# Optimization experiments

Hardware: AMD Instinct MI355X
Metric: run time of the kernel (lower is better)

## Reference

```python
import jax, jax.numpy as jnp
import numpy as np

N, E, D, Z, EA = 25000, 400000, 32, 128, 4


def _mlp(h, W1, b1, W2, b2):
    # MLP_ALL_ACT: activation after every Linear layer
    h = jax.nn.relu(h @ W1 + b1)
    return jax.nn.relu(h @ W2 + b2)


def _super_edge_conv(x, src, dst, edge_attr,
                     eW1, eb1, eW2, eb2, lW1, lb1, lW2, lb2, residual):
    xi = x[dst]            # [E, F] target node features (PyG x_i)
    xj = x[src]            # [E, F] source node features (PyG x_j)
    d = xj - xi
    p = xj * xi
    e1 = jnp.linalg.norm(d, axis=-1, keepdims=True)   # [E, 1]
    e2 = jnp.sum(p, axis=-1, keepdims=True)           # [E, 1]
    feat = jnp.concatenate([xi, d, p, e1, e2, edge_attr], axis=-1)  # [E, 3F+2+EA]
    m = _mlp(feat, eW1, eb1, eW2, eb2)                # [E, Z]
    agg = jax.ops.segment_max(m, dst, num_segments=x.shape[0])  # max aggr per dst node
    agg = jnp.where(jnp.isfinite(agg), agg, 0.0)      # PyG fills empty segments with 0
    y = _mlp(jnp.concatenate([x, agg], axis=-1), lW1, lb1, lW2, lb2)
    return y + x if residual else y


def setup_inputs() -> dict:
    key = jax.random.key(0)
    keys = iter(jax.random.split(key, 64))

    def xav(din, dout):
        s = float(np.sqrt(2.0 / (din + dout)))
        return jax.random.normal(next(keys), (din, dout), jnp.float32) * s

    inp = {}
    inp["x"] = jax.random.normal(next(keys), (N, D), jnp.float32)
    inp["edge_index"] = jax.random.randint(next(keys), (2, E), 0, N)
    inp["edge_attr"] = jax.random.normal(next(keys), (E, EA), jnp.float32)

    def conv_params(prefix, fin):
        e_in = 3 * fin + 2 + EA
        inp[prefix + "_eW1"] = xav(e_in, Z); inp[prefix + "_eb1"] = jnp.zeros((Z,), jnp.float32)
        inp[prefix + "_eW2"] = xav(Z, Z);    inp[prefix + "_eb2"] = jnp.zeros((Z,), jnp.float32)
        inp[prefix + "_lW1"] = xav(fin + Z, Z); inp[prefix + "_lb1"] = jnp.zeros((Z,), jnp.float32)
        inp[prefix + "_lW2"] = xav(Z, Z);    inp[prefix + "_lb2"] = jnp.zeros((Z,), jnp.float32)

    conv_params("c1", D)
    conv_params("c2", Z)
    conv_params("c3", Z)
    inp["fus_W1"] = xav(3 * Z, 2 * Z); inp["fus_b1"] = jnp.zeros((2 * Z,), jnp.float32)
    inp["fus_W2"] = xav(2 * Z, Z);     inp["fus_b2"] = jnp.zeros((Z,), jnp.float32)
    return inp


def reference(x, edge_index, edge_attr,
              c1_eW1, c1_eb1, c1_eW2, c1_eb2, c1_lW1, c1_lb1, c1_lW2, c1_lb2,
              c2_eW1, c2_eb1, c2_eW2, c2_eb2, c2_lW1, c2_lb1, c2_lW2, c2_lb2,
              c3_eW1, c3_eb1, c3_eW2, c3_eb2, c3_lW1, c3_lb1, c3_lW2, c3_lb2,
              fus_W1, fus_b1, fus_W2, fus_b2):
    src, dst = edge_index[0], edge_index[1]
    x1 = _super_edge_conv(x, src, dst, edge_attr,
                          c1_eW1, c1_eb1, c1_eW2, c1_eb2,
                          c1_lW1, c1_lb1, c1_lW2, c1_lb2, residual=False)
    x2 = _super_edge_conv(x1, src, dst, edge_attr,
                          c2_eW1, c2_eb1, c2_eW2, c2_eb2,
                          c2_lW1, c2_lb1, c2_lW2, c2_lb2, residual=True)
    x3 = _super_edge_conv(x2, src, dst, edge_attr,
                          c3_eW1, c3_eb1, c3_eW2, c3_eb2,
                          c3_lW1, c3_lb1, c3_lW2, c3_lb2, residual=True)
    return _mlp(jnp.concatenate([x1, x2, x3], axis=-1), fus_W1, fus_b1, fus_W2, fus_b2)
```

## Files before the change

kernel.cpp:

```cpp
#include <hip/hip_runtime.h>
#include <math.h>

#define DEV __device__ __forceinline__

typedef __attribute__((ext_vector_type(8))) short bf16x8;
typedef __attribute__((ext_vector_type(4))) float f32x4;

DEV short f2bf(float v) {
    union { float f; unsigned u; } c; c.f = v;
    unsigned r = c.u + 0x7fffu + ((c.u >> 16) & 1u);
    return (short)(r >> 16);
}
DEV float bf2f(short s) {
    return __uint_as_float(((unsigned)(unsigned short)s) << 16);
}
DEV unsigned cvt_pk(float lo, float hi) {
    unsigned r;
    asm("v_cvt_pk_bf16_f32 %0, %1, %2" : "=v"(r) : "v"(lo), "v"(hi));
    return r;
}
DEV uint2 pk4(const float4 v) {
    uint2 r; r.x = cvt_pk(v.x, v.y); r.y = cvt_pk(v.z, v.w); return r;
}

#define NPACK 20
struct PackJobs {
    const float* W[NPACK];
    const float* Wsub[NPACK];
    int KIN[NPACK];
    int NOUT[NPACK];
    int end[NPACK];
};

__global__ __launch_bounds__(256)
void pack_all(PackJobs j, short* __restrict__ out, int total)
{
    const int idx = blockIdx.x * 256 + threadIdx.x;
    if (idx >= total) return;
    int job = 0;
    while (idx >= j.end[job]) ++job;
    const int base = job ? j.end[job - 1] : 0;
    const int w = idx - base;
    const int nout = j.NOUT[job];
    const int per_ks = nout * 32;
    const int ks = w / per_ks;
    const int r  = w - ks * per_ks;
    const int n  = r >> 5;
    const int kg = (r >> 3) & 3;
    const int i  = r & 7;
    const int k  = ks * 32 + kg * 8 + i;
    float val = 0.0f;
    if (k < j.KIN[job]) {
        val = j.W[job][(size_t)k * nout + n];
        if (j.Wsub[job]) val -= j.Wsub[job][(size_t)k * nout + n];
    }
    out[idx] = f2bf(val);
}

__global__ __launch_bounds__(256)
void hist_kernel(const int* __restrict__ dst, int* __restrict__ cnt, int E)
{
    const int e = blockIdx.x * 256 + threadIdx.x;
    if (e < E) atomicAdd(&cnt[dst[e]], 1);
}

__global__ __launch_bounds__(1024)
void scan_kernel(int* __restrict__ cnt, int NB)
{
    __shared__ int part[1024];
    const int t = threadIdx.x;
    const int CH = (NB + 1023) >> 10;
    const int base = t * CH;
    int s = 0;
    for (int k = 0; k < CH; ++k) { const int i = base + k; if (i < NB) s += cnt[i]; }
    part[t] = s;
    __syncthreads();
    for (int off = 1; off < 1024; off <<= 1) {
        const int add = (t >= off) ? part[t - off] : 0;
        __syncthreads();
        part[t] += add;
        __syncthreads();
    }
    int run = part[t] - s;
    for (int k = 0; k < CH; ++k) {
        const int i = base + k;
        if (i < NB) { const int c = cnt[i]; cnt[i] = run; run += c; }
    }
}

__global__ __launch_bounds__(256)
void scatter_kernel(const int* __restrict__ src, const int* __restrict__ dst,
                    const float* __restrict__ ea, int* __restrict__ cursor,
                    int* __restrict__ sSrc, int* __restrict__ sDst,
                    short* __restrict__ eaB, int E)
{
    const int e = blockIdx.x * 256 + threadIdx.x;
    if (e >= E) return;
    const int d = dst[e];
    const int p = atomicAdd(&cursor[d], 1);
    sSrc[p] = src[e];
    sDst[p] = d;
    const float4 a = ((const float4*)ea)[e];
    *(uint2*)(eaB + (size_t)p * 4) = pk4(a);
}

template<int KP, int FSTR, int NOUT, bool BIAS>
DEV void mfma_gemm(const short* aLds, const short* __restrict__ Wpk,
                   const float* __restrict__ b, int row0, int c0, int lane,
                   f32x4 (&acc)[8])
{
    const int l15 = lane & 15;
    const int lg  = lane >> 4;
#pragma unroll
    for (int f = 0; f < 8; ++f) {
        if (BIAS) {
            const float bv = b[c0 + f * 16 + l15];
            acc[f] = (f32x4){bv, bv, bv, bv};
        } else {
            acc[f] = (f32x4){0.f, 0.f, 0.f, 0.f};
        }
    }
    const short* arow  = aLds + (row0 + l15) * FSTR + lg * 8;
    const short* wbase = Wpk + (size_t)(c0 + l15) * 32 + lg * 8;
#pragma unroll
    for (int ks = 0; ks < KP / 32; ++ks) {
        const bf16x8 av = *(const bf16x8*)(arow + ks * 32);
        const short* wp = wbase + (size_t)ks * NOUT * 32;
#pragma unroll
        for (int f = 0; f < 8; ++f) {
            const bf16x8 bv = *(const bf16x8*)(wp + f * 512);
            acc[f] = __builtin_amdgcn_mfma_f32_16x16x32_bf16(av, bv, acc[f], 0, 0, 0);
        }
    }
}

template<int OSTR>
DEV void pack_relu(const f32x4 (&acc)[8], short* out, int row0, int c0, int lane)
{
    const int l15 = lane & 15;
    const int lg  = lane >> 4;
#pragma unroll
    for (int f = 0; f < 8; ++f)
#pragma unroll
        for (int i = 0; i < 4; ++i) {
            const int row = row0 + lg * 4 + i;
            const int col = c0 + f * 16 + l15;
            const float vv = fmaxf(acc[f][i], 0.0f);
            const float o = __shfl_xor(vv, 1);
            if (!(lane & 1))
                *(unsigned*)&out[row * OSTR + col] = cvt_pk(vv, o);
        }
}

DEV void store_bf16(const f32x4 (&acc)[8], short* __restrict__ out,
                    int n0, int wave, int lane, int N)
{
    const int l15 = lane & 15;
    const int lg  = lane >> 4;
#pragma unroll
    for (int f = 0; f < 8; ++f)
#pragma unroll
        for (int i = 0; i < 4; ++i) {
            const float vv = acc[f][i];
            const float o = __shfl_xor(vv, 1);
            if (!(lane & 1)) {
                const int n = n0 + wave * 16 + lg * 4 + i;
                if (n < N)
                    *(unsigned*)&out[(size_t)n * 128 + f * 16 + l15] = cvt_pk(vv, o);
            }
        }
}

template<int FIN, int FSTR>
__global__ __launch_bounds__(256)
void uv_pre(const float* __restrict__ xin,
            const short* __restrict__ Wd, const float* __restrict__ b1,
            const short* __restrict__ Wb,
            short* __restrict__ uB, short* __restrict__ vB,
            float* __restrict__ sq, short* __restrict__ xB, int N)
{
    __shared__ __align__(16) short feat[64 * FSTR];
    const int tid = threadIdx.x, lane = tid & 63, wave = tid >> 6;
    const int n0 = blockIdx.x * 64;
    {
        const int r = tid >> 2, s = tid & 3, n = n0 + r;
        short* frow = feat + r * FSTR;
        if (n < N) {
            const float4* xr = (const float4*)(xin + (size_t)n * FIN);
            float ss = 0.f;
#pragma unroll
            for (int d4 = s; d4 < FIN / 4; d4 += 4) {
                const float4 a = xr[d4];
                ss += a.x * a.x + a.y * a.y + a.z * a.z + a.w * a.w;
                const uint2 sv = pk4(a);
                *(uint2*)(frow + d4 * 4) = sv;
                *(uint2*)(xB + (size_t)n * FIN + d4 * 4) = sv;
            }
            ss += __shfl_xor(ss, 1); ss += __shfl_xor(ss, 2);
            if (s == 0) sq[n] = ss;
        } else {
            for (int d = s * 4; d < FIN; d += 16) *(short4*)(frow + d) = make_short4(0, 0, 0, 0);
        }
    }
    asm volatile("s_waitcnt lgkmcnt(0)" ::: "memory");
    f32x4 acc[8];
    mfma_gemm<FIN, FSTR, 128, true>(feat, Wd, b1, wave * 16, 0, lane, acc);
    store_bf16(acc, uB, n0, wave, lane, N);
    mfma_gemm<FIN, FSTR, 128, false>(feat, Wb, nullptr, wave * 16, 0, lane, acc);
    store_bf16(acc, vB, n0, wave, lane, N);
}

template<int FIN>
__global__ __launch_bounds__(512, 8)
void edge_conv7(const short* __restrict__ xB,
                const int* __restrict__ sSrc, const int* __restrict__ sDst,
                const short* __restrict__ eaB, const float* __restrict__ sq,
                const short* __restrict__ uB, const short* __restrict__ vB,
                const short* __restrict__ W1pk, const short* __restrict__ W2pk,
                const float* __restrict__ b2,
                float* __restrict__ agg, int E, int swzQ, int swzR)
{
    constexpr int KPP  = FIN + 32;
    constexpr int FSTR = KPP + 8;
    constexpr int H1STR = 136;
    __shared__ __align__(16) short feat[64 * FSTR];
    __shared__ __align__(16) short h1s[64 * H1STR];
    __shared__ int dstv[64];
    const int tid = threadIdx.x, lane = tid & 63, wave = tid >> 6;
    const int l15 = lane & 15, lg = lane >> 4;
    int bid = blockIdx.x;
    {
        const int xcd = bid & 7, idx = bid >> 3;
        bid = (xcd < swzR ? xcd * (swzQ + 1)
                          : swzR * (swzQ + 1) + (xcd - swzR) * swzQ) + idx;
    }
    const int e0 = bid * 64;
    const int c0 = wave * 16;

    {
        const int r = tid >> 3, s = tid & 7, e = e0 + r;
        short* frow = feat + r * FSTR;
        short* urow = h1s + r * H1STR;
        if (e < E) {
            const int si = sSrc[e], di = sDst[e];
            if (s == 0) dstv[r] = di;
            float sp = 0.f;
#pragma unroll
            for (int c = s; c < FIN / 8; c += 8) {
                const bf16x8 a = *(const bf16x8*)(xB + (size_t)si * FIN + c * 8);
                const bf16x8 b = *(const bf16x8*)(xB + (size_t)di * FIN + c * 8);
                float p[8];
#pragma unroll
                for (int jj = 0; jj < 8; ++jj) {
                    p[jj] = bf2f(a[jj]) * bf2f(b[jj]);
                    sp += p[jj];
                }
                uint4 w;
                w.x = cvt_pk(p[0], p[1]); w.y = cvt_pk(p[2], p[3]);
                w.z = cvt_pk(p[4], p[5]); w.w = cvt_pk(p[6], p[7]);
                *(uint4*)(frow + c * 8) = w;
            }
            sp += __shfl_xor(sp, 1); sp += __shfl_xor(sp, 2); sp += __shfl_xor(sp, 4);
            if (s == 0) {
                const float e1v = sqrtf(fmaxf(sq[si] + sq[di] - 2.f * sp, 0.f));
                *(unsigned*)(frow + FIN) = cvt_pk(e1v, sp);
            }
            if (s == 1) {
                const short4 ea = *(const short4*)(eaB + (size_t)e * 4);
                *(short2*)(frow + FIN + 2) = make_short2(ea.x, ea.y);
                *(short2*)(frow + FIN + 4) = make_short2(ea.z, ea.w);
            }
            for (int d = FIN + 6 + s; d < KPP; d += 8) frow[d] = 0;
#pragma unroll
            for (int c = s; c < 16; c += 8) {
                const bf16x8 uu = *(const bf16x8*)(uB + (size_t)di * 128 + c * 8);
                const bf16x8 vv = *(const bf16x8*)(vB + (size_t)si * 128 + c * 8);
                float o[8];
#pragma unroll
                for (int jj = 0; jj < 8; ++jj)
                    o[jj] = bf2f(uu[jj]) + bf2f(vv[jj]);
                uint4 w;
                w.x = cvt_pk(o[0], o[1]); w.y = cvt_pk(o[2], o[3]);
                w.z = cvt_pk(o[4], o[5]); w.w = cvt_pk(o[6], o[7]);
                *(uint4*)(urow + c * 8) = w;
            }
        } else {
            if (s == 0) dstv[r] = -1;
            for (int d = s * 4; d < KPP; d += 32) *(short4*)(frow + d) = make_short4(0, 0, 0, 0);
            for (int d = s * 4; d < 128; d += 32) *(short4*)(urow + d) = make_short4(0, 0, 0, 0);
        }
    }
    __syncthreads();

    f32x4 acc[4];
#pragma unroll
    for (int sb = 0; sb < 4; ++sb) acc[sb] = (f32x4){0.f, 0.f, 0.f, 0.f};
    {
        const short* wb = W1pk + (size_t)(c0 + l15) * 32 + lg * 8;
#pragma unroll
        for (int ks = 0; ks < KPP / 32; ++ks) {
            const bf16x8 bv = *(const bf16x8*)(wb + (size_t)ks * 4096);
#pragma unroll
            for (int sb = 0; sb < 4; ++sb) {
                const bf16x8 av =
                    *(const bf16x8*)(feat + (sb * 16 + l15) * FSTR + ks * 32 + lg * 8);
                acc[sb] = __builtin_amdgcn_mfma_f32_16x16x32_bf16(av, bv, acc[sb], 0, 0, 0);
            }
        }
    }
#pragma unroll
    for (int sb = 0; sb < 4; ++sb)
#pragma unroll
        for (int i = 0; i < 4; ++i) {
            const int row = sb * 16 + lg * 4 + i;
            const int col = c0 + l15;
            float vv = acc[sb][i] + bf2f(h1s[row * H1STR + col]);
            vv = fmaxf(vv, 0.0f);
            const float o = __shfl_xor(vv, 1);
            if (!(lane & 1))
                *(unsigned*)&h1s[row * H1STR + col] = cvt_pk(vv, o);
        }
    __syncthreads();

    {
        const float bv0 = b2[c0 + l15];
#pragma unroll
        for (int sb = 0; sb < 4; ++sb) acc[sb] = (f32x4){bv0, bv0, bv0, bv0};
    }
    {
        const short* wb = W2pk + (size_t)(c0 + l15) * 32 + lg * 8;
#pragma unroll
        for (int ks = 0; ks < 4; ++ks) {
            const bf16x8 bv = *(const bf16x8*)(wb + (size_t)ks * 4096);
#pragma unroll
            for (int sb = 0; sb < 4; ++sb) {
                const bf16x8 av =
                    *(const bf16x8*)(h1s + (sb * 16 + l15) * H1STR + ks * 32 + lg * 8);
                acc[sb] = __builtin_amdgcn_mfma_f32_16x16x32_bf16(av, bv, acc[sb], 0, 0, 0);
            }
        }
    }
    __syncthreads();

#pragma unroll
    for (int sb = 0; sb < 4; ++sb)
#pragma unroll
        for (int i = 0; i < 4; ++i) {
            const int row = sb * 16 + lg * 4 + i;
            const int col = c0 + l15;
            const float vv = fmaxf(acc[sb][i], 0.0f);
            const float o = __shfl_xor(vv, 1);
            if (!(lane & 1))
                *(unsigned*)&h1s[row * H1STR + col] = cvt_pk(vv, o);
        }
    __syncthreads();

    {
        const int c  = tid & 127;
        const int rh = tid >> 7;
        int cur = -1;
        float mx = 0.0f;
#pragma unroll 4
        for (int i2 = 0; i2 < 16; ++i2) {
            const int row = rh * 16 + i2;
            const int d = dstv[row];
            const float val = bf2f(h1s[row * H1STR + c]);
            if (d != cur) {
                if (cur >= 0 && mx > 0.f)
                    atomicMax((int*)agg + (size_t)cur * 128 + c, __float_as_int(mx));
                cur = d;
                mx = val;
            } else {
                mx = fmaxf(mx, val);
            }
        }
        if (cur >= 0 && mx > 0.f)
            atomicMax((int*)agg + (size_t)cur * 128 + c, __float_as_int(mx));
    }
}

template<int FIN, int KP, int FSTR, bool RES>
__global__ __launch_bounds__(256)
void node_mfma(const float* __restrict__ xin, const float* __restrict__ agg,
               const short* __restrict__ W1pk, const float* __restrict__ b1,
               const short* __restrict__ W2pk, const float* __restrict__ b2,
               float* __restrict__ out, int N)
{
    constexpr int H1STR = 136;
    __shared__ __align__(16) short sh[64 * FSTR + 64 * H1STR];
    short* feat = sh;
    short* h1s  = sh + 64 * FSTR;
    const int tid = threadIdx.x, lane = tid & 63, wave = tid >> 6;
    const int n0 = blockIdx.x * 64;

    {
        const int r = tid >> 2, s = tid & 3, n = n0 + r;
        short* frow = feat + r * FSTR;
        if (n < N) {
            const float4* xr = (const float4*)(xin + (size_t)n * FIN);
            const float4* ar = (const float4*)(agg + (size_t)n * 128);
#pragma unroll
            for (int d4 = s; d4 < FIN / 4; d4 += 4)
                *(uint2*)(frow + d4 * 4) = pk4(xr[d4]);
#pragma unroll
            for (int d4 = s; d4 < 32; d4 += 4)
                *(uint2*)(frow + FIN + d4 * 4) = pk4(ar[d4]);
        } else {
            for (int d = s * 4; d < KP; d += 16) *(short4*)(frow + d) = make_short4(0, 0, 0, 0);
        }
    }
    asm volatile("s_waitcnt lgkmcnt(0)" ::: "memory");

    f32x4 acc[8];
    mfma_gemm<KP, FSTR, 128, true>(feat, W1pk, b1, wave * 16, 0, lane, acc);
    pack_relu<H1STR>(acc, h1s, wave * 16, 0, lane);
    asm volatile("s_waitcnt lgkmcnt(0)" ::: "memory");
    mfma_gemm<128, H1STR, 128, true>(h1s, W2pk, b2, wave * 16, 0, lane, acc);
    {
        const int l15 = lane & 15, lg = lane >> 4;
#pragma unroll
        for (int f = 0; f < 8; ++f)
#pragma unroll
            for (int i = 0; i < 4; ++i) {
                const int n = n0 + wave * 16 + lg * 4 + i;
                if (n < N) {
                    const int c = f * 16 + l15;
                    float v = fmaxf(acc[f][i], 0.0f);
                    if (RES) v += xin[(size_t)n * 128 + c];
                    out[(size_t)n * 128 + c] = v;
                }
            }
    }
}

__global__ __launch_bounds__(128)
void fusion_mfma(const float* __restrict__ x1, const float* __restrict__ x2,
                 const float* __restrict__ x3,
                 const short* __restrict__ W1pk, const float* __restrict__ b1,
                 const short* __restrict__ W2pk, const float* __restrict__ b2,
                 float* __restrict__ out, int N)
{
    constexpr int FSTR = 392;
    constexpr int H1STR = 264;
    __shared__ __align__(16) short sh[32 * FSTR + 32 * H1STR];
    short* feat = sh;
    short* h1s  = sh + 32 * FSTR;
    const int tid = threadIdx.x, lane = tid & 63, wave = tid >> 6;
    const int n0 = blockIdx.x * 32;

    {
        const int r = tid >> 2, s = tid & 3, n = n0 + r;
        short* frow = feat + r * FSTR;
        if (n < N) {
            const float4* a1 = (const float4*)(x1 + (size_t)n * 128);
            const float4* a2 = (const float4*)(x2 + (size_t)n * 128);
            const float4* a3 = (const float4*)(x3 + (size_t)n * 128);
#pragma unroll
            for (int d4 = s; d4 < 32; d4 += 4) {
                *(uint2*)(frow + d4 * 4)       = pk4(a1[d4]);
                *(uint2*)(frow + 128 + d4 * 4) = pk4(a2[d4]);
                *(uint2*)(frow + 256 + d4 * 4) = pk4(a3[d4]);
            }
        } else {
            for (int d = s * 4; d < 384; d += 16) *(short4*)(frow + d) = make_short4(0, 0, 0, 0);
        }
    }
    asm volatile("s_waitcnt lgkmcnt(0)" ::: "memory");

    f32x4 acc[8];
#pragma unroll
    for (int c0 = 0; c0 < 256; c0 += 128) {
        mfma_gemm<384, FSTR, 256, true>(feat, W1pk, b1, wave * 16, c0, lane, acc);
        pack_relu<H1STR>(acc, h1s, wave * 16, c0, lane);
    }
    asm volatile("s_waitcnt lgkmcnt(0)" ::: "memory");
    mfma_gemm<256, H1STR, 128, true>(h1s, W2pk, b2, wave * 16, 0, lane, acc);
    {
        const int l15 = lane & 15, lg = lane >> 4;
#pragma unroll
        for (int f = 0; f < 8; ++f)
#pragma unroll
            for (int i = 0; i < 4; ++i) {
                const int n = n0 + wave * 16 + lg * 4 + i;
                if (n < N)
                    out[(size_t)n * 128 + f * 16 + l15] = fmaxf(acc[f][i], 0.0f);
            }
    }
}

extern "C" void kernel_launch(void* const* d_in, const int* in_sizes, int n_in,
                              void* d_out, int out_size, void* d_ws, size_t ws_size,
                              hipStream_t stream)
{
    const float* x    = (const float*)d_in[0];
    const int*   eidx = (const int*)d_in[1];
    const float* ea   = (const float*)d_in[2];

    const float* c1_eW1 = (const float*)d_in[3];
    const float* c1_eb1 = (const float*)d_in[4];
    const float* c1_eW2 = (const float*)d_in[5];
    const float* c1_eb2 = (const float*)d_in[6];
    const float* c1_lW1 = (const float*)d_in[7];
    const float* c1_lb1 = (const float*)d_in[8];
    const float* c1_lW2 = (const float*)d_in[9];
    const float* c1_lb2 = (const float*)d_in[10];

    const float* c2_eW1 = (const float*)d_in[11];
    const float* c2_eb1 = (const float*)d_in[12];
    const float* c2_eW2 = (const float*)d_in[13];
    const float* c2_eb2 = (const float*)d_in[14];
    const float* c2_lW1 = (const float*)d_in[15];
    const float* c2_lb1 = (const float*)d_in[16];
    const float* c2_lW2 = (const float*)d_in[17];
    const float* c2_lb2 = (const float*)d_in[18];

    const float* c3_eW1 = (const float*)d_in[19];
    const float* c3_eb1 = (const float*)d_in[20];
    const float* c3_eW2 = (const float*)d_in[21];
    const float* c3_eb2 = (const float*)d_in[22];
    const float* c3_lW1 = (const float*)d_in[23];
    const float* c3_lb1 = (const float*)d_in[24];
    const float* c3_lW2 = (const float*)d_in[25];
    const float* c3_lb2 = (const float*)d_in[26];

    const float* fus_W1 = (const float*)d_in[27];
    const float* fus_b1 = (const float*)d_in[28];
    const float* fus_W2 = (const float*)d_in[29];
    const float* fus_b2 = (const float*)d_in[30];

    const int N = in_sizes[0] / 32;
    const int E = in_sizes[1] / 2;
    const int* srcI = eidx;
    const int* dstI = eidx + E;

    const size_t NP = (size_t)N * 128;
    float* ws  = (float*)d_ws;
    float* x1  = ws;
    float* x2  = x1 + NP;
    float* x3  = x2 + NP;
    float* agg = x3 + NP;
    float* sq  = agg + NP;
    int* cursor = (int*)(sq + N);
    int* sSrc   = cursor + 25024;
    int* sDst   = sSrc + E;
    short* eaB  = (short*)(sDst + E);
    short* uB   = eaB + (size_t)E * 4;
    short* vB   = uB + NP;
    short* xB   = vB + NP;
    short* wpk  = xB + NP;

    short* e1Wd = wpk + 0;
    short* e1Wb = wpk + 4096;
    short* e1Wp = wpk + 8192;
    short* e1W2 = wpk + 16384;
    short* e2Wd = wpk + 32768;
    short* e2Wb = wpk + 49152;
    short* e2Wp = wpk + 65536;
    short* e2W2 = wpk + 86016;
    short* e3Wd = wpk + 102400;
    short* e3Wb = wpk + 118784;
    short* e3Wp = wpk + 135168;
    short* e3W2 = wpk + 155648;
    short* n1W1 = wpk + 172032;
    short* n1W2 = wpk + 192512;
    short* n2W1 = wpk + 208896;
    short* n2W2 = wpk + 241664;
    short* n3W1 = wpk + 258048;
    short* n3W2 = wpk + 290816;
    short* fW1  = wpk + 307200;
    short* fW2  = wpk + 405504;
    const int packTotal = 438272;

    PackJobs pj;
    const float* pw[NPACK] = {
        c1_eW1, c1_eW1 + 32 * 128, c1_eW1 + 64 * 128, c1_eW2,
        c2_eW1, c2_eW1 + 128 * 128, c2_eW1 + 256 * 128, c2_eW2,
        c3_eW1, c3_eW1 + 128 * 128, c3_eW1 + 256 * 128, c3_eW2,
        c1_lW1, c1_lW2, c2_lW1, c2_lW2, c3_lW1, c3_lW2,
        fus_W1, fus_W2};
    const float* ps[NPACK] = {
        c1_eW1 + 32 * 128, nullptr, nullptr, nullptr,
        c2_eW1 + 128 * 128, nullptr, nullptr, nullptr,
        c3_eW1 + 128 * 128, nullptr, nullptr, nullptr,
        nullptr, nullptr, nullptr, nullptr, nullptr, nullptr,
        nullptr, nullptr};
    const int pk_kin[NPACK]  = {32, 32, 38, 128, 128, 128, 134, 128,
                                128, 128, 134, 128, 160, 128, 256, 128, 256, 128,
                                384, 256};
    const int pk_nout[NPACK] = {128, 128, 128, 128, 128, 128, 128, 128,
                                128, 128, 128, 128, 128, 128, 128, 128, 128, 128,
                                256, 128};
    const int pk_end[NPACK]  = {4096, 8192, 16384, 32768, 49152, 65536, 86016, 102400,
                                118784, 135168, 155648, 172032, 192512, 208896, 241664,
                                258048, 290816, 307200, 405504, 438272};
    for (int i = 0; i < NPACK; ++i) {
        pj.W[i] = pw[i]; pj.Wsub[i] = ps[i];
        pj.KIN[i] = pk_kin[i]; pj.NOUT[i] = pk_nout[i]; pj.end[i] = pk_end[i];
    }
    pack_all<<<(packTotal + 255) / 256, 256, 0, stream>>>(pj, wpk, packTotal);

    const int eblk = (E + 255) / 256;
    hipMemsetAsync(cursor, 0, 25024 * sizeof(int), stream);
    hist_kernel<<<eblk, 256, 0, stream>>>(dstI, cursor, E);
    scan_kernel<<<1, 1024, 0, stream>>>(cursor, N);
    scatter_kernel<<<eblk, 256, 0, stream>>>(srcI, dstI, ea, cursor, sSrc, sDst, eaB, E);

    const int eblocks = (E + 63) / 64;
    const int nblocks = (N + 63) / 64;
    const int fblocks = (N + 31) / 32;
    const int swzQ = eblocks / 8, swzR = eblocks % 8;
    const size_t aggBytes = NP * sizeof(float);

    uv_pre<32, 40><<<nblocks, 256, 0, stream>>>(x, e1Wd, c1_eb1, e1Wb, uB, vB, sq, xB, N);
    hipMemsetAsync(agg, 0, aggBytes, stream);
    edge_conv7<32><<<eblocks, 512, 0, stream>>>(
        xB, sSrc, sDst, eaB, sq, uB, vB, e1Wp, e1W2, c1_eb2, agg, E, swzQ, swzR);
    node_mfma<32, 160, 168, false><<<nblocks, 256, 0, stream>>>(
        x, agg, n1W1, c1_lb1, n1W2, c1_lb2, x1, N);

    uv_pre<128, 136><<<nblocks, 256, 0, stream>>>(x1, e2Wd, c2_eb1, e2Wb, uB, vB, sq, xB, N);
    hipMemsetAsync(agg, 0, aggBytes, stream);
    edge_conv7<128><<<eblocks, 512, 0, stream>>>(
        xB, sSrc, sDst, eaB, sq, uB, vB, e2Wp, e2W2, c2_eb2, agg, E, swzQ, swzR);
    node_mfma<128, 256, 264, true><<<nblocks, 256, 0, stream>>>(
        x1, agg, n2W1, c2_lb1, n2W2, c2_lb2, x2, N);

    uv_pre<128, 136><<<nblocks, 256, 0, stream>>>(x2, e3Wd, c3_eb1, e3Wb, uB, vB, sq, xB, N);
    hipMemsetAsync(agg, 0, aggBytes, stream);
    edge_conv7<128><<<eblocks, 512, 0, stream>>>(
        xB, sSrc, sDst, eaB, sq, uB, vB, e3Wp, e3W2, c3_eb2, agg, E, swzQ, swzR);
    node_mfma<128, 256, 264, true><<<nblocks, 256, 0, stream>>>(
        x2, agg, n3W1, c3_lb1, n3W2, c3_lb2, x3, N);

    fusion_mfma<<<fblocks, 128, 0, stream>>>(
        x1, x2, x3, fW1, fus_b1, fW2, fus_b2, (float*)d_out, N);
}
```

Measured before the change: 512.8 us.

## Fuse node MLP with next layer's uv precompute and final fusion MLP

Merges each node-update kernel with the following layer's per-node precompute (u/v projections, squared norms, bf16 copy), so the new node features stay in shared memory instead of being reloaded. The third node MLP is fused into the fusion MLP, which removes the x3 buffer and one launch. In edge_conv it reuses the feat buffer for the second-layer output when the stride allows, dropping one block barrier. The cost is more shared memory and register pressure per block, and node_fusion runs with 32-row tiles where the old node kernel used 64.

```diff
diff --git a/kernel.cpp b/kernel.cpp
--- a/kernel.cpp
+++ b/kernel.cpp
@@ -212,7 +212,7 @@
 
 template<int FIN>
 __global__ __launch_bounds__(512, 8)
-void edge_conv7(const short* __restrict__ xB,
+void edge_conv8(const short* __restrict__ xB,
                 const int* __restrict__ sSrc, const int* __restrict__ sDst,
                 const short* __restrict__ eaB, const float* __restrict__ sq,
                 const short* __restrict__ uB, const short* __restrict__ vB,
@@ -223,6 +223,8 @@
     constexpr int KPP  = FIN + 32;
     constexpr int FSTR = KPP + 8;
     constexpr int H1STR = 136;
+    constexpr bool MBF = (FSTR >= 132);
+    constexpr int MS = MBF ? FSTR : H1STR;
     __shared__ __align__(16) short feat[64 * FSTR];
     __shared__ __align__(16) short h1s[64 * H1STR];
     __shared__ int dstv[64];
@@ -340,8 +342,8 @@
             }
         }
     }
-    __syncthreads();
-
+    short* mb = MBF ? feat : h1s;
+    if (!MBF) __syncthreads();
 #pragma unroll
     for (int sb = 0; sb < 4; ++sb)
 #pragma unroll
@@ -351,7 +353,7 @@
             const float vv = fmaxf(acc[sb][i], 0.0f);
             const float o = __shfl_xor(vv, 1);
             if (!(lane & 1))
-                *(unsigned*)&h1s[row * H1STR + col] = cvt_pk(vv, o);
+                *(unsigned*)&mb[row * MS + col] = cvt_pk(vv, o);
         }
     __syncthreads();
 
@@ -364,7 +366,7 @@
         for (int i2 = 0; i2 < 16; ++i2) {
             const int row = rh * 16 + i2;
             const int d = dstv[row];
-            const float val = bf2f(h1s[row * H1STR + c]);
+            const float val = bf2f(mb[row * MS + c]);
             if (d != cur) {
                 if (cur >= 0 && mx > 0.f)
                     atomicMax((int*)agg + (size_t)cur * 128 + c, __float_as_int(mx));
@@ -381,16 +383,21 @@
 
 template<int FIN, int KP, int FSTR, bool RES>
 __global__ __launch_bounds__(256)
-void node_mfma(const float* __restrict__ xin, const float* __restrict__ agg,
-               const short* __restrict__ W1pk, const float* __restrict__ b1,
-               const short* __restrict__ W2pk, const float* __restrict__ b2,
-               float* __restrict__ out, int N)
+void node_uv(const float* __restrict__ xin, const float* __restrict__ agg,
+             const short* __restrict__ W1pk, const float* __restrict__ b1,
+             const short* __restrict__ W2pk, const float* __restrict__ b2,
+             float* __restrict__ out,
+             const short* __restrict__ WdN, const float* __restrict__ b1N,
+             const short* __restrict__ WbN,
+             short* __restrict__ uB, short* __restrict__ vB,
+             float* __restrict__ sq, short* __restrict__ xB, int N)
 {
     constexpr int H1STR = 136;
     __shared__ __align__(16) short sh[64 * FSTR + 64 * H1STR];
     short* feat = sh;
     short* h1s  = sh + 64 * FSTR;
     const int tid = threadIdx.x, lane = tid & 63, wave = tid >> 6;
+    const int l15 = lane & 15, lg = lane >> 4;
     const int n0 = blockIdx.x * 64;
 
     {
@@ -416,76 +423,143 @@
     pack_relu<H1STR>(acc, h1s, wave * 16, 0, lane);
     asm volatile("s_waitcnt lgkmcnt(0)" ::: "memory");
     mfma_gemm<128, H1STR, 128, true>(h1s, W2pk, b2, wave * 16, 0, lane, acc);
-    {
-        const int l15 = lane & 15, lg = lane >> 4;
+
+    {
+        float ss[4] = {0.f, 0.f, 0.f, 0.f};
 #pragma unroll
         for (int f = 0; f < 8; ++f)
 #pragma unroll
             for (int i = 0; i < 4; ++i) {
                 const int n = n0 + wave * 16 + lg * 4 + i;
-                if (n < N) {
-                    const int c = f * 16 + l15;
-                    float v = fmaxf(acc[f][i], 0.0f);
-                    if (RES) v += xin[(size_t)n * 128 + c];
-                    out[(size_t)n * 128 + c] = v;
+                const int c = f * 16 + l15;
+                float v = fmaxf(acc[f][i], 0.0f);
+                if (RES && n < N) v += xin[(size_t)n * 128 + c];
+                if (n < N) out[(size_t)n * 128 + c] = v;
+                ss[i] += v * v;
+                const float o = __shfl_xor(v, 1);
+                if (!(lane & 1)) {
+                    const unsigned pk = cvt_pk(v, o);
+                    const int row = wave * 16 + lg * 4 + i;
+                    *(unsigned*)&h1s[row * H1STR + c] = pk;
+                    if (n < N) *(unsigned*)&xB[(size_t)n * 128 + c] = pk;
                 }
             }
-    }
+#pragma unroll
+        for (int i = 0; i < 4; ++i) {
+            ss[i] += __shfl_xor(ss[i], 1);
+            ss[i] += __shfl_xor(ss[i], 2);
+            ss[i] += __shfl_xor(ss[i], 4);
+            ss[i] += __shfl_xor(ss[i], 8);
+            const int n = n0 + wave * 16 + lg * 4 + i;
+            if (l15 == 0 && n < N) sq[n] = ss[i];
+        }
+    }
+    asm volatile("s_waitcnt lgkmcnt(0)" ::: "memory");
+
+    mfma_gemm<128, H1STR, 128, true>(h1s, WdN, b1N, wave * 16, 0, lane, acc);
+    store_bf16(acc, uB, n0, wave, lane, N);
+    mfma_gemm<128, H1STR, 128, false>(h1s, WbN, nullptr, wave * 16, 0, lane, acc);
+    store_bf16(acc, vB, n0, wave, lane, N);
 }
 
 __global__ __launch_bounds__(128)
-void fusion_mfma(const float* __restrict__ x1, const float* __restrict__ x2,
-                 const float* __restrict__ x3,
+void node_fusion(const float* __restrict__ x1, const float* __restrict__ x2,
+                 const float* __restrict__ agg,
                  const short* __restrict__ W1pk, const float* __restrict__ b1,
                  const short* __restrict__ W2pk, const float* __restrict__ b2,
+                 const short* __restrict__ fW1, const float* __restrict__ fb1,
+                 const short* __restrict__ fW2, const float* __restrict__ fb2,
                  float* __restrict__ out, int N)
 {
-    constexpr int FSTR = 392;
-    constexpr int H1STR = 264;
-    __shared__ __align__(16) short sh[32 * FSTR + 32 * H1STR];
-    short* feat = sh;
-    short* h1s  = sh + 32 * FSTR;
+    constexpr int NSTR = 264;
+    constexpr int H1N  = 136;
+    constexpr int FSF  = 392;
+    constexpr int H1F  = 264;
+    __shared__ __align__(16) short sh[32 * FSF + 32 * H1F];
+    short* featN = sh;
+    short* h1N   = sh + 32 * FSF;
+    short* featF = sh;
+    short* h1F   = sh + 32 * FSF;
     const int tid = threadIdx.x, lane = tid & 63, wave = tid >> 6;
+    const int l15 = lane & 15, lg = lane >> 4;
     const int n0 = blockIdx.x * 32;
 
     {
         const int r = tid >> 2, s = tid & 3, n = n0 + r;
-        short* frow = feat + r * FSTR;
+        short* frow = featN + r * NSTR;
+        if (n < N) {
+            const float4* xr = (const float4*)(x2 + (size_t)n * 128);
+            const float4* ar = (const float4*)(agg + (size_t)n * 128);
+#pragma unroll
+            for (int d4 = s; d4 < 32; d4 += 4) {
+                *(uint2*)(frow + d4 * 4)       = pk4(xr[d4]);
+                *(uint2*)(frow + 128 + d4 * 4) = pk4(ar[d4]);
+            }
+        } else {
+            for (int d = s * 4; d < 256; d += 16) *(short4*)(frow + d) = make_short4(0, 0, 0, 0);
+        }
+    }
+    asm volatile("s_waitcnt lgkmcnt(0)" ::: "memory");
+
+    f32x4 acc[8];
+    mfma_gemm<256, NSTR, 128, true>(featN, W1pk, b1, wave * 16, 0, lane, acc);
+    pack_relu<H1N>(acc, h1N, wave * 16, 0, lane);
+    asm volatile("s_waitcnt lgkmcnt(0)" ::: "memory");
+    mfma_gemm<128, H1N, 128, true>(h1N, W2pk, b2, wave * 16, 0, lane, acc);
+#pragma unroll
+    for (int f = 0; f < 8; ++f)
+#pragma unroll
+        for (int i = 0; i < 4; ++i) {
+            const int n = n0 + wave * 16 + lg * 4 + i;
+            float v = fmaxf(acc[f][i], 0.0f);
+            if (n < N) v += x2[(size_t)n * 128 + f * 16 + l15];
+            acc[f][i] = v;
+        }
+    __syncthreads();
+
+    {
+        const int r = tid >> 2, s = tid & 3, n = n0 + r;
+        short* frow = featF + r * FSF;
         if (n < N) {
             const float4* a1 = (const float4*)(x1 + (size_t)n * 128);
             const float4* a2 = (const float4*)(x2 + (size_t)n * 128);
-            const float4* a3 = (const float4*)(x3 + (size_t)n * 128);
 #pragma unroll
             for (int d4 = s; d4 < 32; d4 += 4) {
                 *(uint2*)(frow + d4 * 4)       = pk4(a1[d4]);
                 *(uint2*)(frow + 128 + d4 * 4) = pk4(a2[d4]);
-                *(uint2*)(frow + 256 + d4 * 4) = pk4(a3[d4]);
             }
         } else {
-            for (int d = s * 4; d < 384; d += 16) *(short4*)(frow + d) = make_short4(0, 0, 0, 0);
-        }
-    }
+            for (int d = s * 4; d < 256; d += 16) *(short4*)(frow + d) = make_short4(0, 0, 0, 0);
+            for (int d = 256 + s * 4; d < 384; d += 16) *(short4*)(frow + d) = make_short4(0, 0, 0, 0);
+        }
+    }
+#pragma unroll
+    for (int f = 0; f < 8; ++f)
+#pragma unroll
+        for (int i = 0; i < 4; ++i) {
+            const int row = wave * 16 + lg * 4 + i;
+            const float v = acc[f][i];
+            const float o = __shfl_xor(v, 1);
+            if (!(lane & 1))
+                *(unsigned*)&featF[row * FSF + 256 + f * 16 + l15] = cvt_pk(v, o);
+        }
     asm volatile("s_waitcnt lgkmcnt(0)" ::: "memory");
 
-    f32x4 acc[8];
 #pragma unroll
     for (int c0 = 0; c0 < 256; c0 += 128) {
-        mfma_gemm<384, FSTR, 256, true>(feat, W1pk, b1, wave * 16, c0, lane, acc);
-        pack_relu<H1STR>(acc, h1s, wave * 16, c0, lane);
+        mfma_gemm<384, FSF, 256, true>(featF, fW1, fb1, wave * 16, c0, lane, acc);
+        pack_relu<H1F>(acc, h1F, wave * 16, c0, lane);
     }
     asm volatile("s_waitcnt lgkmcnt(0)" ::: "memory");
-    mfma_gemm<256, H1STR, 128, true>(h1s, W2pk, b2, wave * 16, 0, lane, acc);
-    {
-        const int l15 = lane & 15, lg = lane >> 4;
-#pragma unroll
-        for (int f = 0; f < 8; ++f)
-#pragma unroll
-            for (int i = 0; i < 4; ++i) {
-                const int n = n0 + wave * 16 + lg * 4 + i;
-                if (n < N)
-                    out[(size_t)n * 128 + f * 16 + l15] = fmaxf(acc[f][i], 0.0f);
-            }
-    }
+    mfma_gemm<256, H1F, 128, true>(h1F, fW2, fb2, wave * 16, 0, lane, acc);
+#pragma unroll
+    for (int f = 0; f < 8; ++f)
+#pragma unroll
+        for (int i = 0; i < 4; ++i) {
+            const int n = n0 + wave * 16 + lg * 4 + i;
+            if (n < N)
+                out[(size_t)n * 128 + f * 16 + l15] = fmaxf(acc[f][i], 0.0f);
+        }
 }
 
 extern "C" void kernel_launch(void* const* d_in, const int* in_sizes, int n_in,
@@ -537,8 +611,7 @@
     float* ws  = (float*)d_ws;
     float* x1  = ws;
     float* x2  = x1 + NP;
-    float* x3  = x2 + NP;
-    float* agg = x3 + NP;
+    float* agg = x2 + NP;
     float* sq  = agg + NP;
     int* cursor = (int*)(sq + N);
     int* sSrc   = cursor + 25024;
@@ -613,25 +686,23 @@
 
     uv_pre<32, 40><<<nblocks, 256, 0, stream>>>(x, e1Wd, c1_eb1, e1Wb, uB, vB, sq, xB, N);
     hipMemsetAsync(agg, 0, aggBytes, stream);
-    edge_conv7<32><<<eblocks, 512, 0, stream>>>(
+    edge_conv8<32><<<eblocks, 512, 0, stream>>>(
         xB, sSrc, sDst, eaB, sq, uB, vB, e1Wp, e1W2, c1_eb2, agg, E, swzQ, swzR);
-    node_mfma<32, 160, 168, false><<<nblocks, 256, 0, stream>>>(
-        x, agg, n1W1, c1_lb1, n1W2, c1_lb2, x1, N);
-
-    uv_pre<128, 136><<<nblocks, 256, 0, stream>>>(x1, e2Wd, c2_eb1, e2Wb, uB, vB, sq, xB, N);
+    node_uv<32, 160, 168, false><<<nblocks, 256, 0, stream>>>(
+        x, agg, n1W1, c1_lb1, n1W2, c1_lb2, x1,
+        e2Wd, c2_eb1, e2Wb, uB, vB, sq, xB, N);
+
     hipMemsetAsync(agg, 0, aggBytes, stream);
-    edge_conv7<128><<<eblocks, 512, 0, stream>>>(
+    edge_conv8<128><<<eblocks, 512, 0, stream>>>(
         xB, sSrc, sDst, eaB, sq, uB, vB, e2Wp, e2W2, c2_eb2, agg, E, swzQ, swzR);
-    node_mfma<128, 256, 264, true><<<nblocks, 256, 0, stream>>>(
-        x1, agg, n2W1, c2_lb1, n2W2, c2_lb2, x2, N);
-
-    uv_pre<128, 136><<<nblocks, 256, 0, stream>>>(x2, e3Wd, c3_eb1, e3Wb, uB, vB, sq, xB, N);
+    node_uv<128, 256, 264, true><<<nblocks, 256, 0, stream>>>(
+        x1, agg, n2W1, c2_lb1, n2W2, c2_lb2, x2,
+        e3Wd, c3_eb1, e3Wb, uB, vB, sq, xB, N);
+
     hipMemsetAsync(agg, 0, aggBytes, stream);
-    edge_conv7<128><<<eblocks, 512, 0, stream>>>(
+    edge_conv8<128><<<eblocks, 512, 0, stream>>>(
         xB, sSrc, sDst, eaB, sq, uB, vB, e3Wp, e3W2, c3_eb2, agg, E, swzQ, swzR);
-    node_mfma<128, 256, 264, true><<<nblocks, 256, 0, stream>>>(
-        x2, agg, n3W1, c3_lb1, n3W2, c3_lb2, x3, N);
-
-    fusion_mfma<<<fblocks, 128, 0, stream>>>(
-        x1, x2, x3, fW1, fus_b1, fW2, fus_b2, (float*)d_out, N);
-}
+    node_fusion<<<fblocks, 128, 0, stream>>>(
+        x1, x2, agg, n3W1, c3_lb1, n3W2, c3_lb2,
+        fW1, fus_b1, fW2, fus_b2, (float*)d_out, N);
+}
```

After: 515.8 us. About the same (+0.6%).
